# Performance work log

Measured on AMD Instinct MI355X. Metric: run time of the kernel, lower is better.

Reference implementation:

```python
import jax, jax.numpy as jnp
import numpy as np

N = 8192        # nodes
D_IN = 512      # input features
H = 256         # hidden (GAT out_features)
D_OUT = 16      # output classes
K = 16          # num clusters/classes
LRELU_SLOPE = 0.2
MASK_FILL = -9e15
EDGE_P = 0.002  # sparsity of random adjacency


def setup_inputs() -> dict:
    key = jax.random.key(0)
    k1, k2, k3, k4, k5, k6 = jax.random.split(key, 6)
    x = jax.random.normal(k1, (N, D_IN), dtype=jnp.float32)
    # binary adjacency with self loops (module only tests adj > 0; support reused as propagation matrix)
    adj = (jax.random.uniform(k2, (N, N)) < EDGE_P).astype(jnp.float32)
    adj = jnp.maximum(adj, jnp.eye(N, dtype=jnp.float32))
    C_a = jax.random.normal(k3, (K, H), dtype=jnp.float32)
    # learned parameters (xavier-ish scale)
    W = jax.random.normal(k4, (D_IN, H), dtype=jnp.float32) * (1.414 * (2.0 / (D_IN + H)) ** 0.5)
    a = jax.random.normal(k5, (2 * H, 1), dtype=jnp.float32) * (1.414 * (2.0 / (2 * H + 1)) ** 0.5)
    W_gcn = jax.random.normal(k6, (H, D_OUT), dtype=jnp.float32)
    return {"x": x, "adj": adj, "C_a": C_a, "W": W, "a": a, "W_gcn": W_gcn}


def _clust_score(Z, C):
    # score[n,k] = exp(-||Z_n - C_k||) normalized over k (beta = 1)
    d = jnp.sqrt(((Z[:, None, :] - C[None, :, :]) ** 2).sum(-1))  # [N,K]
    s = jnp.exp(-d) + 1e-10
    return s / s.sum(axis=1, keepdims=True)


def reference(x, adj, C_a, W, a, W_gcn):
    h = W.shape[1]
    # --- GAT layer ---
    Wh = x @ W                                   # [N,H]
    Wh1 = Wh @ a[:h, :]                          # [N,1]
    Wh2 = Wh @ a[h:, :]                          # [N,1]
    e = jax.nn.leaky_relu(Wh1 + Wh2.T, LRELU_SLOPE)   # [N,N]
    att = jax.nn.softmax(jnp.where(adj > 0, e, MASK_FILL), axis=1)
    Z_0 = att @ Wh                               # h_prime, [N,H]
    gatoutput = jax.nn.elu(Z_0)
    # --- cluster score on detached Z_0 (update=False path) ---
    score = _clust_score(jax.lax.stop_gradient(Z_0), C_a)
    # --- GCN layer (B_1 = I, so Z_1 = F_1) ---
    F_1 = jax.nn.relu(adj @ (gatoutput @ W_gcn))  # [N,D_OUT]
    output = F_1
    Z_1 = F_1
    return (output, Z_1, Z_0, score)
```

## Files before the change

kernel.cpp:

```cpp
#include <hip/hip_runtime.h>
#include <hip/hip_bf16.h>

#define N_NODES 8192
#define D_IN    512
#define H       256
#define D_OUT   16
#define K_CL    16
#define MAXN    96

#define OUT_OFF 0
#define Z1_OFF  131072
#define Z0_OFF  262144
#define SC_OFF  2359296

typedef unsigned int   u32;
typedef unsigned short u16;
typedef __attribute__((ext_vector_type(8))) short bf16x8;
typedef __attribute__((ext_vector_type(4))) float f32x4;

__device__ __forceinline__ float load_in(const void* p, int bf, size_t idx) {
    if (bf) { u32 w = ((const u16*)p)[idx]; return __uint_as_float(w << 16); }
    return ((const float*)p)[idx];
}
__device__ __forceinline__ void store_out(void* p, int bf, size_t idx, float v) {
    if (bf) ((__hip_bfloat16*)p)[idx] = __float2bfloat16(v);
    else    ((float*)p)[idx] = v;
}
__device__ __forceinline__ int detect_bf(const void* adj) {
    return ((const u32*)adj)[0] != 0x3F800000u;
}
__device__ __forceinline__ float bf2f(u32 h) { return __uint_as_float(h << 16); }

__global__ __launch_bounds__(256) void k_prep(
    const void* __restrict__ wraw, const void* av, const void* C_a, const void* Wgcn,
    const void* __restrict__ adj,
    u16* __restrict__ Wt, float* a_f, float* Ca_f, float* Wg_f)
{
    int bf = detect_bf(adj);
    int b = blockIdx.x, tid = threadIdx.x;
    if (b >= 32) {
        int i = (b - 32) * 256 + tid;
        if (i < 512)        a_f[i]         = load_in(av,   bf, i);
        else if (i < 4608)  Ca_f[i - 512]  = load_in(C_a,  bf, i - 512);
        else if (i < 8704)  Wg_f[i - 4608] = load_in(Wgcn, bf, i - 4608);
        return;
    }
    __shared__ float tile[64][65];
    int k0 = (b >> 2) * 64, h0 = (b & 3) * 64;
    int hh = tid & 63, kk = tid >> 6;
    #pragma unroll
    for (int p = 0; p < 16; p++) {
        int k = kk * 16 + p;
        tile[k][hh] = load_in(wraw, bf, (size_t)(k0 + k) * H + h0 + hh);
    }
    __syncthreads();
    int kc = tid & 63, hr = tid >> 6;
    #pragma unroll
    for (int p = 0; p < 16; p++) {
        int h = hr * 16 + p;
        __hip_bfloat16 bb = __float2bfloat16(tile[kc][h]);
        Wt[(size_t)(h0 + h) * D_IN + k0 + kc] = *(u16*)&bb;
    }
}

__global__ __launch_bounds__(256) void k_gemm_wh(
    const void* __restrict__ xraw, const void* __restrict__ wraw,
    const u16* __restrict__ Wt, const void* __restrict__ adj,
    float* __restrict__ Wh, u16* __restrict__ Whb)
{
    int bf = detect_bf(adj);
    __shared__ float xs[32][68];
    __shared__ float ws_[32][68];
    int tid = threadIdx.x;
    int bm = blockIdx.x >> 2, bn = blockIdx.x & 3;
    int m0 = bm * 64, n0 = bn * 64;

    if (bf) {
        int wave = tid >> 6, lane = tid & 63;
        int wr = wave >> 1, wc = wave & 1;
        int r0 = m0 + wr * 32, c0 = n0 + wc * 32;
        int lr = lane & 15, lk = lane >> 4;
        const u16* xp = (const u16*)xraw;
        const u16* a0p = xp + (size_t)(r0 + lr)      * D_IN + lk * 8;
        const u16* a1p = xp + (size_t)(r0 + 16 + lr) * D_IN + lk * 8;
        const u16* b0p = Wt + (size_t)(c0 + lr)      * D_IN + lk * 8;
        const u16* b1p = Wt + (size_t)(c0 + 16 + lr) * D_IN + lk * 8;
        f32x4 acc[2][2] = {};
        #pragma unroll 4
        for (int k0 = 0; k0 < D_IN; k0 += 32) {
            bf16x8 a0 = *(const bf16x8*)(a0p + k0);
            bf16x8 a1 = *(const bf16x8*)(a1p + k0);
            bf16x8 b0 = *(const bf16x8*)(b0p + k0);
            bf16x8 b1 = *(const bf16x8*)(b1p + k0);
            acc[0][0] = __builtin_amdgcn_mfma_f32_16x16x32_bf16(a0, b0, acc[0][0], 0, 0, 0);
            acc[0][1] = __builtin_amdgcn_mfma_f32_16x16x32_bf16(a0, b1, acc[0][1], 0, 0, 0);
            acc[1][0] = __builtin_amdgcn_mfma_f32_16x16x32_bf16(a1, b0, acc[1][0], 0, 0, 0);
            acc[1][1] = __builtin_amdgcn_mfma_f32_16x16x32_bf16(a1, b1, acc[1][1], 0, 0, 0);
        }
        #pragma unroll
        for (int i = 0; i < 2; i++) {
            #pragma unroll
            for (int reg = 0; reg < 4; reg++) {
                int r = r0 + 16 * i + 4 * lk + reg;
                float v0 = acc[i][0][reg], v1 = acc[i][1][reg];
                Wh[(size_t)r * H + c0 + lr]      = v0;
                Wh[(size_t)r * H + c0 + 16 + lr] = v1;
                __hip_bfloat16 h0 = __float2bfloat16(v0), h1 = __float2bfloat16(v1);
                Whb[(size_t)r * H + c0 + lr]      = *(u16*)&h0;
                Whb[(size_t)r * H + c0 + 16 + lr] = *(u16*)&h1;
            }
        }
        return;
    }

    int tx = tid & 15, ty = tid >> 4;
    float acc[4][4] = {};
    for (int k0 = 0; k0 < D_IN; k0 += 32) {
        {
            int r = tid >> 2, kq = (tid & 3) * 8;
            size_t base = (size_t)(m0 + r) * D_IN + k0 + kq;
            float4 f0 = *(const float4*)((const float*)xraw + base);
            float4 f1 = *(const float4*)((const float*)xraw + base + 4);
            xs[kq + 0][r] = f0.x; xs[kq + 1][r] = f0.y;
            xs[kq + 2][r] = f0.z; xs[kq + 3][r] = f0.w;
            xs[kq + 4][r] = f1.x; xs[kq + 5][r] = f1.y;
            xs[kq + 6][r] = f1.z; xs[kq + 7][r] = f1.w;
        }
        {
            int kk = tid >> 3, n8 = (tid & 7) * 8;
            size_t base = (size_t)(k0 + kk) * H + n0 + n8;
            float4 f0 = *(const float4*)((const float*)wraw + base);
            float4 f1 = *(const float4*)((const float*)wraw + base + 4);
            ws_[kk][n8+0]=f0.x; ws_[kk][n8+1]=f0.y; ws_[kk][n8+2]=f0.z; ws_[kk][n8+3]=f0.w;
            ws_[kk][n8+4]=f1.x; ws_[kk][n8+5]=f1.y; ws_[kk][n8+6]=f1.z; ws_[kk][n8+7]=f1.w;
        }
        __syncthreads();
        #pragma unroll
        for (int kk = 0; kk < 32; kk++) {
            float4 a4 = *(const float4*)&xs[kk][ty * 4];
            float4 b4 = *(const float4*)&ws_[kk][tx * 4];
            float a[4] = {a4.x, a4.y, a4.z, a4.w};
            float b[4] = {b4.x, b4.y, b4.z, b4.w};
            #pragma unroll
            for (int i = 0; i < 4; i++)
                #pragma unroll
                for (int j = 0; j < 4; j++)
                    acc[i][j] += a[i] * b[j];
        }
        __syncthreads();
    }
    #pragma unroll
    for (int i = 0; i < 4; i++) {
        float4 o = {acc[i][0], acc[i][1], acc[i][2], acc[i][3]};
        *(float4*)&Wh[(size_t)(m0 + ty*4 + i) * H + n0 + tx*4] = o;
    }
}

__global__ __launch_bounds__(256) void k_wh12(
    const float* __restrict__ Wh, const float* __restrict__ a_f,
    float* __restrict__ Wh1, float* __restrict__ Wh2)
{
    int tid = threadIdx.x;
    int wave = tid >> 6, lane = tid & 63;
    int n = blockIdx.x * 4 + wave;
    float4 v  = *(const float4*)(Wh + (size_t)n * H + lane * 4);
    float4 a1 = *(const float4*)(a_f + lane * 4);
    float4 a2 = *(const float4*)(a_f + H + lane * 4);
    float s1 = v.x*a1.x + v.y*a1.y + v.z*a1.z + v.w*a1.w;
    float s2 = v.x*a2.x + v.y*a2.y + v.z*a2.z + v.w*a2.w;
    #pragma unroll
    for (int off = 32; off; off >>= 1) {
        s1 += __shfl_xor(s1, off);
        s2 += __shfl_xor(s2, off);
    }
    if (lane == 0) { Wh1[n] = s1; Wh2[n] = s2; }
}

__global__ __launch_bounds__(256) void k_gat_row(
    const void* __restrict__ adjraw,
    const float* __restrict__ Wh, const u16* __restrict__ Whb,
    const float* __restrict__ Wh1, const float* __restrict__ Wh2,
    const float* __restrict__ Ca_f, const float* __restrict__ Wg_f,
    float* __restrict__ Gf,
    int* __restrict__ nbr_cnt, u16* __restrict__ nbr_idx,
    void* __restrict__ dout)
{
    const int tid = threadIdx.x;
    const int w = tid >> 6, lane = tid & 63;
    const int n = blockIdx.x * 4 + w;
    const int bf = detect_bf(adjraw);

    __shared__ int   s_cnt[4];
    __shared__ int   s_idx[4][MAXN];
    __shared__ float s_z[4][H];
    __shared__ float s_g[4][H];

    if (lane == 0) s_cnt[w] = 0;

    if (bf) {
        const u16* arow = (const u16*)adjraw + (size_t)n * N_NODES;
        #pragma unroll
        for (int rnd = 0; rnd < 2; rnd++) {
            uint4 r[8];
            #pragma unroll
            for (int it = 0; it < 8; it++)
                r[it] = *(const uint4*)(arow + rnd * 4096 + it * 512 + lane * 8);
            #pragma unroll
            for (int it = 0; it < 8; it++) {
                u32 w4[4] = {r[it].x, r[it].y, r[it].z, r[it].w};
                int base = rnd * 4096 + it * 512 + lane * 8;
                #pragma unroll
                for (int q = 0; q < 4; q++) {
                    if (w4[q]) {
                        if (w4[q] & 0xFFFFu) {
                            int p = atomicAdd(&s_cnt[w], 1);
                            if (p < MAXN) s_idx[w][p] = base + q * 2;
                        }
                        if (w4[q] >> 16) {
                            int p = atomicAdd(&s_cnt[w], 1);
                            if (p < MAXN) s_idx[w][p] = base + q * 2 + 1;
                        }
                    }
                }
            }
        }
    } else {
        const u32* arow = (const u32*)adjraw + (size_t)n * N_NODES;
        #pragma unroll
        for (int rnd = 0; rnd < 4; rnd++) {
            uint4 r[8];
            #pragma unroll
            for (int it = 0; it < 8; it++)
                r[it] = *(const uint4*)(arow + rnd * 2048 + it * 256 + lane * 4);
            #pragma unroll
            for (int it = 0; it < 8; it++) {
                u32 w4[4] = {r[it].x, r[it].y, r[it].z, r[it].w};
                int base = rnd * 2048 + it * 256 + lane * 4;
                #pragma unroll
                for (int q = 0; q < 4; q++) {
                    if (w4[q]) {
                        int p = atomicAdd(&s_cnt[w], 1);
                        if (p < MAXN) s_idx[w][p] = base + q;
                    }
                }
            }
        }
    }
    __syncthreads();
    const int cnt = min(s_cnt[w], MAXN);
    if (lane == 0) nbr_cnt[n] = cnt;
    int i1 = 0, i2 = 0;
    if (lane < cnt)      i1 = s_idx[w][lane];
    if (lane + 64 < cnt) i2 = s_idx[w][lane + 64];
    if (lane < cnt)      nbr_idx[(size_t)n * MAXN + lane]      = (u16)i1;
    if (lane + 64 < cnt) nbr_idx[(size_t)n * MAXN + lane + 64] = (u16)i2;

    const float wh1n = Wh1[n];
    float e1 = -3e38f, e2 = -3e38f;
    if (lane < cnt)      { float v = wh1n + Wh2[i1]; e1 = v > 0.f ? v : 0.2f * v; }
    if (lane + 64 < cnt) { float v = wh1n + Wh2[i2]; e2 = v > 0.f ? v : 0.2f * v; }
    float m = fmaxf(e1, e2);
    #pragma unroll
    for (int off = 32; off; off >>= 1) m = fmaxf(m, __shfl_xor(m, off));
    float x1 = (lane < cnt)      ? expf(e1 - m) : 0.f;
    float x2 = (lane + 64 < cnt) ? expf(e2 - m) : 0.f;
    float ssum = x1 + x2;
    #pragma unroll
    for (int off = 32; off; off >>= 1) ssum += __shfl_xor(ssum, off);
    float inv = 1.f / ssum;
    float at1 = x1 * inv, at2 = x2 * inv;

    const int c4 = lane * 4;
    float az[4] = {0.f, 0.f, 0.f, 0.f};
    if (bf) {
        int t = 0;
        for (; t + 4 <= cnt; t += 4) {
            int ja[4]; float wa[4];
            #pragma unroll
            for (int u = 0; u < 4; u++) {
                int tt = t + u;
                ja[u] = __shfl((tt < 64) ? i1 : i2, tt & 63);
                wa[u] = __shfl((tt < 64) ? at1 : at2, tt & 63);
            }
            uint2 rr[4];
            #pragma unroll
            for (int u = 0; u < 4; u++)
                rr[u] = *(const uint2*)(Whb + (size_t)ja[u] * H + c4);
            #pragma unroll
            for (int u = 0; u < 4; u++) {
                az[0] += wa[u] * bf2f(rr[u].x & 0xFFFFu);
                az[1] += wa[u] * bf2f(rr[u].x >> 16);
                az[2] += wa[u] * bf2f(rr[u].y & 0xFFFFu);
                az[3] += wa[u] * bf2f(rr[u].y >> 16);
            }
        }
        for (; t < cnt; t++) {
            int   it_ = __shfl((t < 64) ? i1 : i2, t & 63);
            float wt_ = __shfl((t < 64) ? at1 : at2, t & 63);
            uint2 r = *(const uint2*)(Whb + (size_t)it_ * H + c4);
            az[0] += wt_ * bf2f(r.x & 0xFFFFu);
            az[1] += wt_ * bf2f(r.x >> 16);
            az[2] += wt_ * bf2f(r.y & 0xFFFFu);
            az[3] += wt_ * bf2f(r.y >> 16);
        }
    } else {
        int t = 0;
        for (; t + 4 <= cnt; t += 4) {
            int ja[4]; float wa[4];
            #pragma unroll
            for (int u = 0; u < 4; u++) {
                int tt = t + u;
                ja[u] = __shfl((tt < 64) ? i1 : i2, tt & 63);
                wa[u] = __shfl((tt < 64) ? at1 : at2, tt & 63);
            }
            float4 rr[4];
            #pragma unroll
            for (int u = 0; u < 4; u++)
                rr[u] = *(const float4*)(Wh + (size_t)ja[u] * H + c4);
            #pragma unroll
            for (int u = 0; u < 4; u++) {
                az[0] += wa[u] * rr[u].x; az[1] += wa[u] * rr[u].y;
                az[2] += wa[u] * rr[u].z; az[3] += wa[u] * rr[u].w;
            }
        }
        for (; t < cnt; t++) {
            int   it_ = __shfl((t < 64) ? i1 : i2, t & 63);
            float wt_ = __shfl((t < 64) ? at1 : at2, t & 63);
            float4 v = *(const float4*)(Wh + (size_t)it_ * H + c4);
            az[0] += wt_ * v.x; az[1] += wt_ * v.y;
            az[2] += wt_ * v.z; az[3] += wt_ * v.w;
        }
    }
    #pragma unroll
    for (int q = 0; q < 4; q++) {
        float z = az[q];
        store_out(dout, bf, (size_t)Z0_OFF + (size_t)n * H + c4 + q, z);
        s_z[w][c4 + q] = z;
        s_g[w][c4 + q] = z > 0.f ? z : expf(z) - 1.f;
    }
    __syncthreads();

    {
        int k = lane & 15, g = lane >> 4;
        const float* cz = &s_z[w][0];
        const float* ck = Ca_f + (size_t)k * H;
        float d2 = 0.f;
        #pragma unroll 8
        for (int i = 0; i < 64; i++) {
            int ch = g * 64 + ((i + g * 16) & 63);
            float d = cz[ch] - ck[ch];
            d2 += d * d;
        }
        d2 += __shfl_xor(d2, 16);
        d2 += __shfl_xor(d2, 32);
        float sc = expf(-sqrtf(d2)) + 1e-10f;
        float tot = sc;
        tot += __shfl_xor(tot, 1); tot += __shfl_xor(tot, 2);
        tot += __shfl_xor(tot, 4); tot += __shfl_xor(tot, 8);
        if (lane < 16)
            store_out(dout, bf, (size_t)SC_OFF + (size_t)n * K_CL + lane, sc / tot);
    }

    {
        int o = lane & 15, g = lane >> 4;
        const float* cg = &s_g[w][0];
        float p = 0.f;
        #pragma unroll 8
        for (int i = 0; i < 64; i++) {
            int ch = g * 64 + ((i + g * 16) & 63);
            p += cg[ch] * Wg_f[(size_t)ch * D_OUT + o];
        }
        p += __shfl_xor(p, 16);
        p += __shfl_xor(p, 32);
        if (lane < 16) Gf[(size_t)n * D_OUT + lane] = p;
    }
}

__global__ __launch_bounds__(256) void k_f1(
    const int* __restrict__ nbr_cnt, const u16* __restrict__ nbr_idx,
    const float* __restrict__ Gf, const void* __restrict__ adj,
    void* __restrict__ dout)
{
    int tid = threadIdx.x;
    int bf = detect_bf(adj);
    int r = tid >> 4, o = tid & 15;
    int n = blockIdx.x * 16 + r;
    int cnt = nbr_cnt[n];
    const u16* idx = nbr_idx + (size_t)n * MAXN;
    float acc = 0.f;
    int t = 0;
    for (; t + 4 <= cnt; t += 4) {
        int i0 = idx[t], i1 = idx[t+1], i2 = idx[t+2], i3 = idx[t+3];
        float g0 = Gf[(size_t)i0 * D_OUT + o];
        float g1 = Gf[(size_t)i1 * D_OUT + o];
        float g2 = Gf[(size_t)i2 * D_OUT + o];
        float g3 = Gf[(size_t)i3 * D_OUT + o];
        acc += g0; acc += g1; acc += g2; acc += g3;
    }
    for (; t < cnt; t++)
        acc += Gf[(size_t)idx[t] * D_OUT + o];
    acc = fmaxf(acc, 0.f);
    store_out(dout, bf, (size_t)OUT_OFF + (size_t)n * D_OUT + o, acc);
    store_out(dout, bf, (size_t)Z1_OFF  + (size_t)n * D_OUT + o, acc);
}

extern "C" void kernel_launch(void* const* d_in, const int* in_sizes, int n_in,
                              void* d_out, int out_size, void* d_ws, size_t ws_size,
                              hipStream_t stream) {
    const void* x    = d_in[0];
    const void* adj  = d_in[1];
    const void* C_a  = d_in[2];
    const void* W    = d_in[3];
    const void* av   = d_in[4];
    const void* Wgcn = d_in[5];

    char* wsp = (char*)d_ws;
    float* Wh   = (float*)wsp;                 wsp += (size_t)N_NODES * H * 4;
    u16*   Whb  = (u16*)wsp;                   wsp += (size_t)N_NODES * H * 2;
    float* Wh1  = (float*)wsp;                 wsp += (size_t)N_NODES * 4;
    float* Wh2  = (float*)wsp;                 wsp += (size_t)N_NODES * 4;
    float* Gf   = (float*)wsp;                 wsp += (size_t)N_NODES * D_OUT * 4;
    int*   ncnt = (int*)wsp;                   wsp += (size_t)N_NODES * 4;
    u16*   nidx = (u16*)wsp;                   wsp += (size_t)N_NODES * MAXN * 2;
    float* a_f  = (float*)wsp;                 wsp += 2 * H * 4;
    float* Ca_f = (float*)wsp;                 wsp += (size_t)K_CL * H * 4;
    float* Wg_f = (float*)wsp;                 wsp += (size_t)H * D_OUT * 4;
    u16*   Wt   = (u16*)wsp;                   wsp += (size_t)H * D_IN * 2;

    k_prep    <<<66, 256, 0, stream>>>(W, av, C_a, Wgcn, adj, Wt, a_f, Ca_f, Wg_f);
    k_gemm_wh <<<512, 256, 0, stream>>>(x, W, Wt, adj, Wh, Whb);
    k_wh12    <<<N_NODES / 4, 256, 0, stream>>>(Wh, a_f, Wh1, Wh2);
    k_gat_row <<<N_NODES / 4, 256, 0, stream>>>(adj, Wh, Whb, Wh1, Wh2, Ca_f, Wg_f,
                                                Gf, ncnt, nidx, d_out);
    k_f1      <<<N_NODES / 16, 256, 0, stream>>>(ncnt, nidx, Gf, adj, d_out);
}
```

Measured before the change: 469.6 us.

## Move adjacency scan into a dedicated fully-coalesced grid-wide kernel with global atomics

Builds the neighbor lists in a separate kernel, k_scan. Every thread reads 16-byte chunks of the whole adjacency matrix in a flat, fully coalesced order and appends column indices to per-row lists with global atomics. Before, each GAT row wave scanned its own adjacency row inside the attention kernel. The aim is to stream the large adjacency read at full bandwidth with high occupancy, kept apart from the compute-heavy GAT kernel. In exchange it adds a memset, an extra launch, and global atomics. Neighbor order within each row also becomes nondeterministic, which can change floating-point summation order.

Result: slower. 507.5 us (+8.1%).

```diff
diff --git a/kernel.cpp b/kernel.cpp
--- a/kernel.cpp
+++ b/kernel.cpp
@@ -60,6 +60,77 @@
         int h = hr * 16 + p;
         __hip_bfloat16 bb = __float2bfloat16(tile[kc][h]);
         Wt[(size_t)(h0 + h) * D_IN + k0 + kc] = *(u16*)&bb;
+    }
+}
+
+__global__ __launch_bounds__(256) void k_scan(
+    const void* __restrict__ adjraw,
+    int* __restrict__ ncnt, u16* __restrict__ nidx)
+{
+    const int bf = detect_bf(adjraw);
+    const int gid = blockIdx.x * 256 + threadIdx.x;
+    const int NT = 2048 * 256;
+    const uint4* A = (const uint4*)adjraw;
+    if (bf) {
+        #pragma unroll
+        for (int g = 0; g < 4; g++) {
+            uint4 r[4];
+            #pragma unroll
+            for (int u = 0; u < 4; u++)
+                r[u] = A[(size_t)(g * 4 + u) * NT + gid];
+            u32 any = 0;
+            #pragma unroll
+            for (int u = 0; u < 4; u++) any |= r[u].x | r[u].y | r[u].z | r[u].w;
+            if (any) {
+                #pragma unroll
+                for (int u = 0; u < 4; u++) {
+                    size_t w0 = ((size_t)(g * 4 + u) * NT + gid) * 8;
+                    u32 ws[4] = {r[u].x, r[u].y, r[u].z, r[u].w};
+                    #pragma unroll
+                    for (int q = 0; q < 4; q++) {
+                        if (ws[q] & 0xFFFFu) {
+                            size_t i = w0 + q * 2;
+                            int row = (int)(i >> 13), col = (int)(i & 8191);
+                            int p = atomicAdd(&ncnt[row], 1);
+                            if (p < MAXN) nidx[(size_t)row * MAXN + p] = (u16)col;
+                        }
+                        if (ws[q] >> 16) {
+                            size_t i = w0 + q * 2 + 1;
+                            int row = (int)(i >> 13), col = (int)(i & 8191);
+                            int p = atomicAdd(&ncnt[row], 1);
+                            if (p < MAXN) nidx[(size_t)row * MAXN + p] = (u16)col;
+                        }
+                    }
+                }
+            }
+        }
+    } else {
+        #pragma unroll
+        for (int g = 0; g < 8; g++) {
+            uint4 r[4];
+            #pragma unroll
+            for (int u = 0; u < 4; u++)
+                r[u] = A[(size_t)(g * 4 + u) * NT + gid];
+            u32 any = 0;
+            #pragma unroll
+            for (int u = 0; u < 4; u++) any |= r[u].x | r[u].y | r[u].z | r[u].w;
+            if (any) {
+                #pragma unroll
+                for (int u = 0; u < 4; u++) {
+                    size_t f0 = ((size_t)(g * 4 + u) * NT + gid) * 4;
+                    u32 ws[4] = {r[u].x, r[u].y, r[u].z, r[u].w};
+                    #pragma unroll
+                    for (int q = 0; q < 4; q++) {
+                        if (ws[q]) {
+                            size_t i = f0 + q;
+                            int row = (int)(i >> 13), col = (int)(i & 8191);
+                            int p = atomicAdd(&ncnt[row], 1);
+                            if (p < MAXN) nidx[(size_t)row * MAXN + p] = (u16)col;
+                        }
+                    }
+                }
+            }
+        }
     }
 }
 
@@ -177,12 +248,11 @@
 }
 
 __global__ __launch_bounds__(256) void k_gat_row(
-    const void* __restrict__ adjraw,
+    const int* __restrict__ ncnt, const u16* __restrict__ nidx,
     const float* __restrict__ Wh, const u16* __restrict__ Whb,
     const float* __restrict__ Wh1, const float* __restrict__ Wh2,
     const float* __restrict__ Ca_f, const float* __restrict__ Wg_f,
-    float* __restrict__ Gf,
-    int* __restrict__ nbr_cnt, u16* __restrict__ nbr_idx,
+    float* __restrict__ Gf, const void* __restrict__ adjraw,
     void* __restrict__ dout)
 {
     const int tid = threadIdx.x;
@@ -190,70 +260,13 @@
     const int n = blockIdx.x * 4 + w;
     const int bf = detect_bf(adjraw);
 
-    __shared__ int   s_cnt[4];
-    __shared__ int   s_idx[4][MAXN];
     __shared__ float s_z[4][H];
     __shared__ float s_g[4][H];
 
-    if (lane == 0) s_cnt[w] = 0;
-
-    if (bf) {
-        const u16* arow = (const u16*)adjraw + (size_t)n * N_NODES;
-        #pragma unroll
-        for (int rnd = 0; rnd < 2; rnd++) {
-            uint4 r[8];
-            #pragma unroll
-            for (int it = 0; it < 8; it++)
-                r[it] = *(const uint4*)(arow + rnd * 4096 + it * 512 + lane * 8);
-            #pragma unroll
-            for (int it = 0; it < 8; it++) {
-                u32 w4[4] = {r[it].x, r[it].y, r[it].z, r[it].w};
-                int base = rnd * 4096 + it * 512 + lane * 8;
-                #pragma unroll
-                for (int q = 0; q < 4; q++) {
-                    if (w4[q]) {
-                        if (w4[q] & 0xFFFFu) {
-                            int p = atomicAdd(&s_cnt[w], 1);
-                            if (p < MAXN) s_idx[w][p] = base + q * 2;
-                        }
-                        if (w4[q] >> 16) {
-                            int p = atomicAdd(&s_cnt[w], 1);
-                            if (p < MAXN) s_idx[w][p] = base + q * 2 + 1;
-                        }
-                    }
-                }
-            }
-        }
-    } else {
-        const u32* arow = (const u32*)adjraw + (size_t)n * N_NODES;
-        #pragma unroll
-        for (int rnd = 0; rnd < 4; rnd++) {
-            uint4 r[8];
-            #pragma unroll
-            for (int it = 0; it < 8; it++)
-                r[it] = *(const uint4*)(arow + rnd * 2048 + it * 256 + lane * 4);
-            #pragma unroll
-            for (int it = 0; it < 8; it++) {
-                u32 w4[4] = {r[it].x, r[it].y, r[it].z, r[it].w};
-                int base = rnd * 2048 + it * 256 + lane * 4;
-                #pragma unroll
-                for (int q = 0; q < 4; q++) {
-                    if (w4[q]) {
-                        int p = atomicAdd(&s_cnt[w], 1);
-                        if (p < MAXN) s_idx[w][p] = base + q;
-                    }
-                }
-            }
-        }
-    }
-    __syncthreads();
-    const int cnt = min(s_cnt[w], MAXN);
-    if (lane == 0) nbr_cnt[n] = cnt;
+    const int cnt = min(ncnt[n], MAXN);
     int i1 = 0, i2 = 0;
-    if (lane < cnt)      i1 = s_idx[w][lane];
-    if (lane + 64 < cnt) i2 = s_idx[w][lane + 64];
-    if (lane < cnt)      nbr_idx[(size_t)n * MAXN + lane]      = (u16)i1;
-    if (lane + 64 < cnt) nbr_idx[(size_t)n * MAXN + lane + 64] = (u16)i2;
+    if (lane < cnt)      i1 = nidx[(size_t)n * MAXN + lane];
+    if (lane + 64 < cnt) i2 = nidx[(size_t)n * MAXN + lane + 64];
 
     const float wh1n = Wh1[n];
     float e1 = -3e38f, e2 = -3e38f;
@@ -385,7 +398,7 @@
     int bf = detect_bf(adj);
     int r = tid >> 4, o = tid & 15;
     int n = blockIdx.x * 16 + r;
-    int cnt = nbr_cnt[n];
+    int cnt = min(nbr_cnt[n], MAXN);
     const u16* idx = nbr_idx + (size_t)n * MAXN;
     float acc = 0.f;
     int t = 0;
@@ -427,10 +440,12 @@
     float* Wg_f = (float*)wsp;                 wsp += (size_t)H * D_OUT * 4;
     u16*   Wt   = (u16*)wsp;                   wsp += (size_t)H * D_IN * 2;
 
+    hipMemsetAsync(ncnt, 0, (size_t)N_NODES * 4, stream);
     k_prep    <<<66, 256, 0, stream>>>(W, av, C_a, Wgcn, adj, Wt, a_f, Ca_f, Wg_f);
+    k_scan    <<<2048, 256, 0, stream>>>(adj, ncnt, nidx);
     k_gemm_wh <<<512, 256, 0, stream>>>(x, W, Wt, adj, Wh, Whb);
     k_wh12    <<<N_NODES / 4, 256, 0, stream>>>(Wh, a_f, Wh1, Wh2);
-    k_gat_row <<<N_NODES / 4, 256, 0, stream>>>(adj, Wh, Whb, Wh1, Wh2, Ca_f, Wg_f,
-                                                Gf, ncnt, nidx, d_out);
+    k_gat_row <<<N_NODES / 4, 256, 0, stream>>>(ncnt, nidx, Wh, Whb, Wh1, Wh2,
+                                                Ca_f, Wg_f, Gf, adj, d_out);
     k_f1      <<<N_NODES / 16, 256, 0, stream>>>(ncnt, nidx, Gf, adj, d_out);
 }
```
